# Performance work log

Measured on AMD Instinct MI355X. Metric: run time of the kernel, lower is better.

## Reference

```python
import jax, jax.numpy as jnp
import numpy as np
from jax import lax

B, T, E, D, CC, K, H = 64, 2000, 512, 1024, 32, 31, 128
PAD = (K - 1) // 2


def setup_inputs() -> dict:
    key = jax.random.key(0)
    ks = jax.random.split(key, 12)
    enc_output = jax.random.normal(ks[0], (B, T, E), dtype=jnp.float32)
    text_len = jax.random.randint(ks[1], (B,), 1, T + 1)
    dec_state = jax.random.normal(ks[2], (B, D), dtype=jnp.float32)
    prev_att_w = jax.random.uniform(ks[3], (B, T), dtype=jnp.float32)
    # learned parameters
    W_enc = jax.random.normal(ks[4], (E, H), dtype=jnp.float32) / np.sqrt(E)
    b_enc = jnp.zeros((H,), dtype=jnp.float32)
    W_dec = jax.random.normal(ks[5], (D, H), dtype=jnp.float32) / np.sqrt(D)
    W_att = jax.random.normal(ks[6], (CC, H), dtype=jnp.float32) / np.sqrt(CC)
    conv_w = jax.random.normal(ks[7], (CC, 1, K), dtype=jnp.float32) / np.sqrt(K)  # OIH
    W_out = jax.random.normal(ks[8], (H, 1), dtype=jnp.float32) / np.sqrt(H)
    b_out = jnp.zeros((1,), dtype=jnp.float32)
    return {
        'enc_output': enc_output, 'text_len': text_len, 'dec_state': dec_state,
        'prev_att_w': prev_att_w, 'W_enc': W_enc, 'b_enc': b_enc, 'W_dec': W_dec,
        'W_att': W_att, 'conv_w': conv_w, 'W_out': W_out, 'b_out': b_out,
    }


def reference(enc_output, text_len, dec_state, prev_att_w,
              W_enc, b_enc, W_dec, W_att, conv_w, W_out, b_out):
    # processed_memory = fc_enc(enc_output): (B,T,H)
    pm = jnp.einsum('bte,eh->bth', enc_output, W_enc) + b_enc
    # location conv: (B,1,T) -> (B,CC,T), same padding, no bias
    att_conv = lax.conv_general_dilated(
        prev_att_w[:, None, :], conv_w, window_strides=(1,),
        padding=[(PAD, PAD)], dimension_numbers=('NCH', 'OIH', 'NCH'))
    # fc_att on channel dim: (B,T,H)
    att_conv = jnp.einsum('bct,ch->bth', att_conv, W_att)
    # fc_dec(dec_state): (B,1,H)
    dec = (dec_state @ W_dec)[:, None, :]
    # energy: (B,T)
    energy = (jnp.tanh(att_conv + pm + dec) @ W_out)[..., 0] + b_out[0]
    att_w = jax.nn.softmax(energy, axis=1)  # (B,T)
    att_c = jnp.einsum('bte,bt->be', enc_output, att_w)  # (B,E)
    return att_c, att_w
```

## Files before the change

### kernel.cpp

```cpp
#include <hip/hip_runtime.h>
#include <hip/hip_fp16.h>

typedef _Float16 f16x8 __attribute__((ext_vector_type(8)));
typedef float f32x4 __attribute__((ext_vector_type(4)));


__device__ __forceinline__ unsigned short f2h(float f) {
  __half h = __float2half(f);
  return __builtin_bit_cast(unsigned short, h);
}

__device__ __forceinline__ f16x8 u4_to_f16x8(uint4 v) {
  return __builtin_bit_cast(f16x8, v);
}

__device__ __forceinline__ float fast_tanh(float x) {
  return 1.f - 2.f / (__expf(2.f * x) + 1.f);
}

__global__ __launch_bounds__(256) void prep_kernel(
    const float* __restrict__ dec_state, const float* __restrict__ W_dec,
    const float* __restrict__ b_enc, const float* __restrict__ conv_w,
    const float* __restrict__ W_att, const float* __restrict__ W_enc,
    float* __restrict__ decb, unsigned short* __restrict__ MTg,
    unsigned short* __restrict__ WTpack)
{
  const int blk = blockIdx.x, tid = threadIdx.x;
  if (blk < 32) {
    __shared__ float sd[2048];
    const int sub = tid >> 7, h = tid & 127;
    const int b = blk*2 + sub;
    for (int i = h; i < 1024; i += 128) sd[sub*1024 + i] = dec_state[b*1024 + i];
    __syncthreads();
    float acc = b_enc[h];
    #pragma unroll 8
    for (int d = 0; d < 1024; ++d) acc = fmaf(sd[sub*1024 + d], W_dec[d*128 + h], acc);
    decb[b*128 + h] = acc;
  } else if (blk < 96) {
    const int e0 = (blk - 32) * 8;
    #pragma unroll
    for (int jj = 0; jj < 4; ++jj) {
      int idx = tid + jj*256;
      int el = idx >> 7, hh = idx & 127;
      int e = e0 + el;
      int kc = e >> 6, ks = (e >> 5) & 1, lg = (e >> 3) & 3, j = e & 7;
      int nt = hh >> 4, lr = hh & 15;
      int dst = (((kc*2 + ks)*8 + nt)*64 + lg*16 + lr)*8 + j;
      WTpack[dst] = f2h(W_enc[e*128 + hh]);
    }
  } else {
    if (tid < 128) {
      const int h = tid;
      for (int k = 0; k < 31; ++k) {
        float a = 0.f;
        #pragma unroll
        for (int c = 0; c < 32; ++c) a = fmaf(conv_w[c*31 + k], W_att[c*128 + h], a);
        MTg[h*32 + k] = f2h(a);
      }
      MTg[h*32 + 31] = 0;
    }
  }
}

__global__ __launch_bounds__(256, 2) void energy_kernel(
    const float* __restrict__ enc, const float* __restrict__ prev,
    const unsigned short* __restrict__ WTpack, const unsigned short* __restrict__ MTg,
    const float* __restrict__ decb, const float* __restrict__ W_out,
    float* __restrict__ energy)
{
  __shared__ __align__(16) unsigned short sFrag[4*16*64*8];
  __shared__ float sPrev[96];
  __shared__ float sDecb[128];
  __shared__ float sWout[128];

  const int b  = blockIdx.y;
  const int t0 = blockIdx.x * 64;
  const int tid = threadIdx.x;
  const int wave = tid >> 6, lane = tid & 63;
  const int lr = lane & 15, lg = lane >> 4;

  if (tid < 128) { sDecb[tid] = decb[b*128 + tid]; sWout[tid] = W_out[tid]; }
  if (tid < 96) {
    int tt = t0 + tid - 15;
    sPrev[tid] = (tt >= 0 && tt < 2000) ? prev[b*2000 + tt] : 0.f;
  }

  const float* encB = enc + (size_t)b * (2000u*512u);

  {
    const int row_half = tid >> 7;
    const int e  = (tid & 127) * 4;
    const int fs = e >> 5;
    const int lge = (e >> 3) & 3;
    const int jh  = e & 7;
    char* sB = (char*)sFrag;
    #pragma unroll 8
    for (int c = 0; c < 32; ++c) {
      int row = 2*c + row_half;
      int tg = t0 + row; if (tg > 1999) tg = 1999;
      float4 v = *reinterpret_cast<const float4*>(encB + (size_t)tg*512 + e);
      int slot = (lge*16 + (row & 15)) ^ fs;
      char* dst = sB + (row >> 4)*16384 + fs*1024 + slot*16 + jh*2;
      uint2 wv;
      wv.x = ((unsigned)f2h(v.y) << 16) | f2h(v.x);
      wv.y = ((unsigned)f2h(v.w) << 16) | f2h(v.z);
      *reinterpret_cast<uint2*>(dst) = wv;
    }
  }
  __syncthreads();

  const char* fbase = (const char*)sFrag + wave*16384;
  const char* wp = (const char*)WTpack + lane*16;

  f32x4 acc[8];
  #pragma unroll
  for (int i = 0; i < 8; ++i) acc[i] = (f32x4){0,0,0,0};

  #pragma unroll
  for (int kc = 0; kc < 8; ++kc) {
    const int fs0 = kc*2, fs1 = kc*2 + 1;
    f16x8 a0 = *reinterpret_cast<const f16x8*>(fbase + fs0*1024 + ((lane ^ fs0) & 63)*16);
    f16x8 a1 = *reinterpret_cast<const f16x8*>(fbase + fs1*1024 + ((lane ^ fs1) & 63)*16);
    #pragma unroll
    for (int nt = 0; nt < 8; ++nt) {
      uint4 rb = *reinterpret_cast<const uint4*>(wp + (fs0*8 + nt)*1024);
      acc[nt] = __builtin_amdgcn_mfma_f32_16x16x32_f16(a0, u4_to_f16x8(rb), acc[nt], 0, 0, 0);
    }
    #pragma unroll
    for (int nt = 0; nt < 8; ++nt) {
      uint4 rb = *reinterpret_cast<const uint4*>(wp + (fs1*8 + nt)*1024);
      acc[nt] = __builtin_amdgcn_mfma_f32_16x16x32_f16(a1, u4_to_f16x8(rb), acc[nt], 0, 0, 0);
    }
  }

  {
    f16x8 a2;
    const int pb0 = wave*16 + lr + lg*8;
    #pragma unroll
    for (int j = 0; j < 8; ++j)
      a2[j] = __builtin_bit_cast(_Float16, f2h(sPrev[pb0 + j]));
    const char* mb = (const char*)MTg + lr*64 + lg*16;
    #pragma unroll
    for (int nt = 0; nt < 8; ++nt) {
      uint4 mv = *reinterpret_cast<const uint4*>(mb + nt*1024);
      acc[nt] = __builtin_amdgcn_mfma_f32_16x16x32_f16(a2, u4_to_f16x8(mv), acc[nt], 0, 0, 0);
    }
  }

  {
    float es0 = 0.f, es1 = 0.f, es2 = 0.f, es3 = 0.f;
    #pragma unroll
    for (int nt = 0; nt < 8; ++nt) {
      float dh = sDecb[nt*16 + lr];
      float wo = sWout[nt*16 + lr];
      es0 += fast_tanh(acc[nt][0] + dh) * wo;
      es1 += fast_tanh(acc[nt][1] + dh) * wo;
      es2 += fast_tanh(acc[nt][2] + dh) * wo;
      es3 += fast_tanh(acc[nt][3] + dh) * wo;
    }
    #pragma unroll
    for (int off = 1; off < 16; off <<= 1) {
      es0 += __shfl_xor(es0, off, 64);
      es1 += __shfl_xor(es1, off, 64);
      es2 += __shfl_xor(es2, off, 64);
      es3 += __shfl_xor(es3, off, 64);
    }
    if (lr == 0) {
      const int t = t0 + wave*16 + lg*4;
      float ev[4] = {es0, es1, es2, es3};
      #pragma unroll
      for (int r = 0; r < 4; ++r)
        if (t + r < 2000) energy[b*2000 + t + r] = ev[r];
    }
  }
}

__global__ __launch_bounds__(256) void softmax_kernel(
    const float* __restrict__ energy, float* __restrict__ attw)
{
  const int b = blockIdx.x, tid = threadIdx.x;
  __shared__ float red[4];
  __shared__ float red2[4];
  float m = -1e30f;
  for (int i = tid; i < 2000; i += 256) m = fmaxf(m, energy[b*2000 + i]);
  #pragma unroll
  for (int off = 1; off < 64; off <<= 1) m = fmaxf(m, __shfl_xor(m, off, 64));
  if ((tid & 63) == 0) red[tid >> 6] = m;
  __syncthreads();
  m = fmaxf(fmaxf(red[0], red[1]), fmaxf(red[2], red[3]));

  float s = 0.f;
  for (int i = tid; i < 2000; i += 256) {
    float p = __expf(energy[b*2000 + i] - m);
    attw[b*2000 + i] = p;
    s += p;
  }
  #pragma unroll
  for (int off = 1; off < 64; off <<= 1) s += __shfl_xor(s, off, 64);
  if ((tid & 63) == 0) red2[tid >> 6] = s;
  __syncthreads();
  s = red2[0] + red2[1] + red2[2] + red2[3];
  float inv = 1.f / s;
  for (int i = tid; i < 2000; i += 256) attw[b*2000 + i] *= inv;
}

__global__ __launch_bounds__(256) void attc_partial_kernel(
    const float* __restrict__ enc, const float* __restrict__ attw,
    float* __restrict__ part)
{
  const int b = blockIdx.y, ch = blockIdx.x, tid = threadIdx.x;
  const int p = tid >> 7;
  const int e4 = (tid & 127) * 4;
  const int tstart = ch * 125 + p, tend = ch * 125 + 125;
  const float* encB = enc + (size_t)b * (2000u*512u);
  float a0 = 0.f, a1 = 0.f, a2 = 0.f, a3 = 0.f;
  #pragma unroll 2
  for (int t = tstart; t < tend; t += 2) {
    float w = attw[b*2000 + t];
    float4 v = *reinterpret_cast<const float4*>(encB + (size_t)t*512 + e4);
    a0 = fmaf(v.x, w, a0);
    a1 = fmaf(v.y, w, a1);
    a2 = fmaf(v.z, w, a2);
    a3 = fmaf(v.w, w, a3);
  }
  float4 out = {a0, a1, a2, a3};
  *reinterpret_cast<float4*>(part + ((size_t)(b*32 + ch*2 + p))*512 + e4) = out;
}

__global__ __launch_bounds__(128) void attc_reduce_kernel(
    const float* __restrict__ part, float* __restrict__ out)
{
  const int b = blockIdx.x, e4 = threadIdx.x * 4;
  float4 s = {0.f, 0.f, 0.f, 0.f};
  #pragma unroll
  for (int c = 0; c < 32; ++c) {
    float4 v = *reinterpret_cast<const float4*>(part + ((size_t)(b*32 + c))*512 + e4);
    s.x += v.x; s.y += v.y; s.z += v.z; s.w += v.w;
  }
  *reinterpret_cast<float4*>(out + b*512 + e4) = s;
}

extern "C" void kernel_launch(void* const* d_in, const int* in_sizes, int n_in,
                              void* d_out, int out_size, void* d_ws, size_t ws_size,
                              hipStream_t stream) {
  (void)in_sizes; (void)n_in; (void)out_size; (void)ws_size;
  const float* enc       = (const float*)d_in[0];
  const float* dec_state = (const float*)d_in[2];
  const float* prev      = (const float*)d_in[3];
  const float* W_enc     = (const float*)d_in[4];
  const float* b_enc     = (const float*)d_in[5];
  const float* W_dec     = (const float*)d_in[6];
  const float* W_att     = (const float*)d_in[7];
  const float* conv_w    = (const float*)d_in[8];
  const float* W_out     = (const float*)d_in[9];

  char* ws = (char*)d_ws;
  float*          energy = (float*)(ws + 0);
  float*          decb   = (float*)(ws + 524288);
  unsigned short* MTg    = (unsigned short*)(ws + 557056);
  unsigned short* WTpack = (unsigned short*)(ws + 565248);
  float*          part   = (float*)(ws + 696320);

  float* attc = (float*)d_out;
  float* attw = (float*)d_out + 64*512;

  prep_kernel        <<<97, 256, 0, stream>>>(dec_state, W_dec, b_enc, conv_w, W_att, W_enc,
                                              decb, MTg, WTpack);
  energy_kernel      <<<dim3(32, 64), 256, 0, stream>>>(enc, prev, WTpack, MTg, decb, W_out, energy);
  softmax_kernel     <<<64, 256, 0, stream>>>(energy, attw);
  attc_partial_kernel<<<dim3(16, 64), 256, 0, stream>>>(enc, attw, part);
  attc_reduce_kernel <<<64, 128, 0, stream>>>(part, attc);
}
```

Measured before the change: 180.9 us.

## Load encoder A-fragments directly from global into registers, drop LDS staging

```diff
diff --git a/kernel.cpp b/kernel.cpp
--- a/kernel.cpp
+++ b/kernel.cpp
@@ -12,6 +12,15 @@
 
 __device__ __forceinline__ f16x8 u4_to_f16x8(uint4 v) {
   return __builtin_bit_cast(f16x8, v);
+}
+
+__device__ __forceinline__ f16x8 cvt8(float4 u, float4 v) {
+  uint4 w;
+  w.x = ((unsigned)f2h(u.y) << 16) | f2h(u.x);
+  w.y = ((unsigned)f2h(u.w) << 16) | f2h(u.z);
+  w.z = ((unsigned)f2h(v.y) << 16) | f2h(v.x);
+  w.w = ((unsigned)f2h(v.w) << 16) | f2h(v.z);
+  return u4_to_f16x8(w);
 }
 
 __device__ __forceinline__ float fast_tanh(float x) {
@@ -62,13 +71,12 @@
   }
 }
 
-__global__ __launch_bounds__(256, 2) void energy_kernel(
+__global__ __launch_bounds__(256, 4) void energy_kernel(
     const float* __restrict__ enc, const float* __restrict__ prev,
     const unsigned short* __restrict__ WTpack, const unsigned short* __restrict__ MTg,
     const float* __restrict__ decb, const float* __restrict__ W_out,
     float* __restrict__ energy)
 {
-  __shared__ __align__(16) unsigned short sFrag[4*16*64*8];
   __shared__ float sPrev[96];
   __shared__ float sDecb[128];
   __shared__ float sWout[128];
@@ -84,53 +92,46 @@
     int tt = t0 + tid - 15;
     sPrev[tid] = (tt >= 0 && tt < 2000) ? prev[b*2000 + tt] : 0.f;
   }
+  __syncthreads();
 
   const float* encB = enc + (size_t)b * (2000u*512u);
-
-  {
-    const int row_half = tid >> 7;
-    const int e  = (tid & 127) * 4;
-    const int fs = e >> 5;
-    const int lge = (e >> 3) & 3;
-    const int jh  = e & 7;
-    char* sB = (char*)sFrag;
-    #pragma unroll 8
-    for (int c = 0; c < 32; ++c) {
-      int row = 2*c + row_half;
-      int tg = t0 + row; if (tg > 1999) tg = 1999;
-      float4 v = *reinterpret_cast<const float4*>(encB + (size_t)tg*512 + e);
-      int slot = (lge*16 + (row & 15)) ^ fs;
-      char* dst = sB + (row >> 4)*16384 + fs*1024 + slot*16 + jh*2;
-      uint2 wv;
-      wv.x = ((unsigned)f2h(v.y) << 16) | f2h(v.x);
-      wv.y = ((unsigned)f2h(v.w) << 16) | f2h(v.z);
-      *reinterpret_cast<uint2*>(dst) = wv;
-    }
-  }
-  __syncthreads();
-
-  const char* fbase = (const char*)sFrag + wave*16384;
+  int tg = t0 + wave*16 + lr; if (tg > 1999) tg = 1999;
+  const float* rowp = encB + (size_t)tg*512 + lg*8;
   const char* wp = (const char*)WTpack + lane*16;
 
   f32x4 acc[8];
   #pragma unroll
   for (int i = 0; i < 8; ++i) acc[i] = (f32x4){0,0,0,0};
 
+  float4 c0 = *reinterpret_cast<const float4*>(rowp + 0);
+  float4 c1 = *reinterpret_cast<const float4*>(rowp + 4);
+  float4 c2 = *reinterpret_cast<const float4*>(rowp + 32);
+  float4 c3 = *reinterpret_cast<const float4*>(rowp + 36);
+
   #pragma unroll
   for (int kc = 0; kc < 8; ++kc) {
-    const int fs0 = kc*2, fs1 = kc*2 + 1;
-    f16x8 a0 = *reinterpret_cast<const f16x8*>(fbase + fs0*1024 + ((lane ^ fs0) & 63)*16);
-    f16x8 a1 = *reinterpret_cast<const f16x8*>(fbase + fs1*1024 + ((lane ^ fs1) & 63)*16);
-    #pragma unroll
-    for (int nt = 0; nt < 8; ++nt) {
-      uint4 rb = *reinterpret_cast<const uint4*>(wp + (fs0*8 + nt)*1024);
-      acc[nt] = __builtin_amdgcn_mfma_f32_16x16x32_f16(a0, u4_to_f16x8(rb), acc[nt], 0, 0, 0);
-    }
-    #pragma unroll
-    for (int nt = 0; nt < 8; ++nt) {
-      uint4 rb = *reinterpret_cast<const uint4*>(wp + (fs1*8 + nt)*1024);
-      acc[nt] = __builtin_amdgcn_mfma_f32_16x16x32_f16(a1, u4_to_f16x8(rb), acc[nt], 0, 0, 0);
-    }
+    uint4 rb0[8], rb1[8];
+    #pragma unroll
+    for (int nt = 0; nt < 8; ++nt)
+      rb0[nt] = *reinterpret_cast<const uint4*>(wp + ((kc*2 + 0)*8 + nt)*1024);
+    #pragma unroll
+    for (int nt = 0; nt < 8; ++nt)
+      rb1[nt] = *reinterpret_cast<const uint4*>(wp + ((kc*2 + 1)*8 + nt)*1024);
+    f16x8 a0 = cvt8(c0, c1);
+    f16x8 a1 = cvt8(c2, c3);
+    if (kc < 7) {
+      const float* p = rowp + (kc+1)*64;
+      c0 = *reinterpret_cast<const float4*>(p + 0);
+      c1 = *reinterpret_cast<const float4*>(p + 4);
+      c2 = *reinterpret_cast<const float4*>(p + 32);
+      c3 = *reinterpret_cast<const float4*>(p + 36);
+    }
+    #pragma unroll
+    for (int nt = 0; nt < 8; ++nt)
+      acc[nt] = __builtin_amdgcn_mfma_f32_16x16x32_f16(a0, u4_to_f16x8(rb0[nt]), acc[nt], 0, 0, 0);
+    #pragma unroll
+    for (int nt = 0; nt < 8; ++nt)
+      acc[nt] = __builtin_amdgcn_mfma_f32_16x16x32_f16(a1, u4_to_f16x8(rb1[nt]), acc[nt], 0, 0, 0);
   }
 
   {
```

After: 220.4 us. 21.8% more time.
